# Kernel optimization log

Measured on AMD Instinct MI355X. Metric: run time of the kernel, lower is better.

Reference implementation:

```python
import jax, jax.numpy as jnp
import numpy as np

B, T, D, UNITS = 64, 1024, 512, 1024

def setup_inputs() -> dict:
    key = jax.random.key(0)
    ks = jax.random.split(key, 8)
    s = lambda fan_in: 1.0 / np.sqrt(fan_in)
    return {
        "features": jax.random.normal(ks[0], (B, T, D), dtype=jnp.float32),
        "hidden": jax.random.normal(ks[1], (B, D), dtype=jnp.float32),
        "W1_w": jax.random.normal(ks[2], (D, UNITS), dtype=jnp.float32) * s(D),
        "W1_b": jnp.zeros((UNITS,), dtype=jnp.float32),
        "W2_w": jax.random.normal(ks[3], (D, UNITS), dtype=jnp.float32) * s(D),
        "W2_b": jnp.zeros((UNITS,), dtype=jnp.float32),
        "V_w": jax.random.normal(ks[4], (UNITS, 1), dtype=jnp.float32) * s(UNITS),
        "V_b": jnp.zeros((1,), dtype=jnp.float32),
    }

def reference(features, hidden, W1_w, W1_b, W2_w, W2_b, V_w, V_b):
    # features: [B,T,D], hidden: [B,D]
    proj_f = jnp.einsum('btd,du->btu', features, W1_w) + W1_b          # [B,T,U]
    proj_h = (hidden @ W2_w + W2_b)[:, None, :]                        # [B,1,U]
    score = jnp.tanh(proj_f + proj_h)                                  # [B,T,U]
    logits = jnp.einsum('btu,uo->bto', score, V_w) + V_b               # [B,T,1]
    attention_weights = jax.nn.softmax(logits, axis=1)                 # [B,T,1]
    context_vector = jnp.sum(attention_weights * features, axis=1)     # [B,D]
    return context_vector, attention_weights
```

## Files before the change

### kernel.cpp

```cpp
#include <hip/hip_runtime.h>
#include <math.h>

#define B_ 64
#define T_ 1024
#define D_ 512
#define U_ 1024

typedef __bf16 bf16x8 __attribute__((ext_vector_type(8)));
typedef float f32x16 __attribute__((ext_vector_type(16)));
typedef unsigned int u32;

__device__ __forceinline__ float fast_tanh(float x) {
    float ax = fabsf(x);
    float e = __expf(2.0f * ax);
    float r = 1.0f - __fdividef(2.0f, e + 1.0f);
    return copysignf(r, x);
}

__device__ __forceinline__ u32 f2bf_pk(float lo, float hi) {
    u32 a = __float_as_uint(lo) + 0x8000u;
    u32 b = __float_as_uint(hi) + 0x8000u;
    return (a >> 16) | (b & 0xffff0000u);
}

__global__ __launch_bounds__(256) void prep_kernel(
    const float* __restrict__ W1, const float* __restrict__ hidden,
    const float* __restrict__ W2, const float* __restrict__ W2b,
    const float* __restrict__ W1b,
    unsigned short* __restrict__ W1F, float* __restrict__ ph,
    float* __restrict__ ctx0) {
    if (blockIdx.x < 256) {
        const int gid  = blockIdx.x * 256 + threadIdx.x;
        const int lane = gid & 63;
        const int frag = gid >> 6;
        const int ks = frag & 1;
        const int kt = (frag >> 1) & 15;
        const int ut = frag >> 5;
        const int u  = ut * 32 + (lane & 31);
        const int k0 = kt * 32 + ks * 16 + (lane >> 5) * 8;
        float f[8];
#pragma unroll
        for (int j = 0; j < 8; ++j) f[j] = W1[(size_t)(k0 + j) * U_ + u];
        uint4 w;
        w.x = f2bf_pk(f[0], f[1]);
        w.y = f2bf_pk(f[2], f[3]);
        w.z = f2bf_pk(f[4], f[5]);
        w.w = f2bf_pk(f[6], f[7]);
        *(uint4*)&W1F[(size_t)gid * 8] = w;
    } else {
        const int bx = blockIdx.x - 256;
        const int zi = bx * 256 + (int)threadIdx.x;
        if (zi < B_ * D_) ctx0[zi] = 0.f;
        const int u  = (bx & 3) * 256 + threadIdx.x;
        const int b  = bx >> 2;
        const float* h = hidden + b * D_;
        float acc = 0.f;
#pragma unroll 8
        for (int d = 0; d < D_; ++d) acc = fmaf(h[d], W2[(size_t)d * U_ + u], acc);
        ph[b * U_ + u] = acc + W2b[u] + W1b[u];
    }
}

__global__ __launch_bounds__(512, 4) void logits_mfma_kernel(
    const float* __restrict__ feat,
    const unsigned short* __restrict__ W1F,
    const float* __restrict__ ph,
    const float* __restrict__ Vw,
    float* __restrict__ lpart) {
    __shared__ __align__(16) char As[65536];

    const int tid  = threadIdx.x;
    const int tt   = blockIdx.x;
    const int b    = blockIdx.y;
    const int t0   = tt * 64;
    const int lane = tid & 63;
    const int widx = tid >> 6;
    const int l31 = lane & 31, g = lane >> 5;

    {
        const int r  = tid >> 3;
        const int s0 = tid & 7;
        const float* src = feat + ((size_t)(b * T_ + t0 + r)) * D_;
        const int xr = (r >> 2) & 3;
#pragma unroll
        for (int i = 0; i < 8; ++i) {
            const int s = s0 + 8 * i;
            const float4 v0 = *(const float4*)(src + s * 8);
            const float4 v1 = *(const float4*)(src + s * 8 + 4);
            uint4 w;
            w.x = f2bf_pk(v0.x, v0.y);
            w.y = f2bf_pk(v0.z, v0.w);
            w.z = f2bf_pk(v1.x, v1.y);
            w.w = f2bf_pk(v1.z, v1.w);
            const int panel = s >> 2, q = s & 3;
            *(uint4*)&As[panel * 4096 + r * 64 + (q ^ xr) * 16] = w;
        }
    }
    __syncthreads();

    const char* bb0 = (const char*)W1F + (size_t)(widx * 2) * 32768 + lane * 16;
    const char* bb1 = bb0 + (size_t)16 * 32768;

    f32x16 acc[2][2];
    bf16x8 b0[4], b1[4];

    auto loadB = [&](const char* bb, bf16x8* dst, int kt) {
#pragma unroll
        for (int nt = 0; nt < 2; ++nt)
#pragma unroll
            for (int ks = 0; ks < 2; ++ks)
                dst[nt * 2 + ks] =
                    *(const bf16x8*)(bb + nt * 32768 + (kt * 2 + ks) * 1024);
    };

    auto computeStep = [&](int kt, const bf16x8* bfr) {
        bf16x8 af[2][2];
#pragma unroll
        for (int ks = 0; ks < 2; ++ks)
#pragma unroll
            for (int mt = 0; mt < 2; ++mt) {
                const int rr = mt * 32 + l31;
                const int q  = (2 * ks + g) ^ ((rr >> 2) & 3);
                af[ks][mt] = *(const bf16x8*)&As[kt * 4096 + rr * 64 + q * 16];
            }
        __builtin_amdgcn_s_setprio(1);
#pragma unroll
        for (int ks = 0; ks < 2; ++ks)
#pragma unroll
            for (int mt = 0; mt < 2; ++mt)
#pragma unroll
                for (int nt = 0; nt < 2; ++nt)
                    acc[mt][nt] = __builtin_amdgcn_mfma_f32_32x32x16_bf16(
                        af[ks][mt], bfr[nt * 2 + ks], acc[mt][nt], 0, 0, 0);
        __builtin_amdgcn_s_setprio(0);
    };

    loadB(bb0, b0, 0);
#pragma unroll
    for (int uh = 0; uh < 2; ++uh) {
        const char* bb = uh ? bb1 : bb0;
#pragma unroll
        for (int mt = 0; mt < 2; ++mt)
#pragma unroll
            for (int nt = 0; nt < 2; ++nt) acc[mt][nt] = (f32x16)(0.f);

        for (int kt = 0; kt < 16; kt += 2) {
            loadB(bb, b1, kt + 1);
            computeStep(kt, b0);
            if (kt + 2 < 16) loadB(bb, b0, kt + 2);
            computeStep(kt + 1, b1);
        }
        if (uh == 0) loadB(bb1, b0, 0);

        float v[32];
#pragma unroll
        for (int i = 0; i < 32; ++i) v[i] = 0.f;

#pragma unroll
        for (int nt = 0; nt < 2; ++nt) {
            const int u = uh * 512 + widx * 64 + nt * 32 + l31;
            const float phv = ph[b * U_ + u];
            const float vw  = Vw[u];
#pragma unroll
            for (int mt = 0; mt < 2; ++mt)
#pragma unroll
                for (int r = 0; r < 16; ++r)
                    v[mt * 16 + r] =
                        fmaf(vw, fast_tanh(acc[mt][nt][r] + phv), v[mt * 16 + r]);
        }

#pragma unroll
        for (int s = 0; s < 5; ++s) {
            const int pb = 1 << s;
            const bool hi = (l31 & pb) != 0;
#pragma unroll
            for (int j = 0; j < (16 >> s); ++j) {
                const float a = v[2 * j];
                const float c = v[2 * j + 1];
                const float keep = hi ? c : a;
                const float send = hi ? a : c;
                v[j] = keep + __shfl_xor(send, pb);
            }
        }

        const int src = ((lane & 3) | (((lane >> 3) & 3) << 2) |
                         (((lane >> 5) & 1) << 4)) + 32 * ((lane >> 2) & 1);
        const float out = __shfl(v[0], src);
        lpart[((size_t)(uh * 8 + widx)) * (B_ * T_) + (size_t)b * T_ + t0 +
              lane] = out;
    }
}

__global__ __launch_bounds__(512) void ctx_kernel(
    const float* __restrict__ feat, const float* __restrict__ lpart,
    float* __restrict__ attn, float* __restrict__ ctx_out) {
    const int b   = blockIdx.y;
    const int seg = blockIdx.x;
    const int tid = threadIdx.x;
    __shared__ float wls[1024];
    __shared__ float redm[8];
    __shared__ float reds[8];

    float v[2];
    float mx = -3.4e38f;
#pragma unroll
    for (int j = 0; j < 2; ++j) {
        const int t = b * T_ + tid + 512 * j;
        float s0 = 0.f, s1 = 0.f;
#pragma unroll
        for (int sl = 0; sl < 8; ++sl) {
            s0 += lpart[(size_t)(2 * sl) * (B_ * T_) + t];
            s1 += lpart[(size_t)(2 * sl + 1) * (B_ * T_) + t];
        }
        v[j] = s0 + s1;
        mx = fmaxf(mx, v[j]);
    }
#pragma unroll
    for (int off = 32; off > 0; off >>= 1) mx = fmaxf(mx, __shfl_xor(mx, off));
    if ((tid & 63) == 0) redm[tid >> 6] = mx;
    __syncthreads();
    mx = fmaxf(fmaxf(fmaxf(redm[0], redm[1]), fmaxf(redm[2], redm[3])),
               fmaxf(fmaxf(redm[4], redm[5]), fmaxf(redm[6], redm[7])));
    float s = 0.f;
#pragma unroll
    for (int j = 0; j < 2; ++j) {
        v[j] = __expf(v[j] - mx);
        s += v[j];
    }
#pragma unroll
    for (int off = 32; off > 0; off >>= 1) s += __shfl_xor(s, off);
    if ((tid & 63) == 0) reds[tid >> 6] = s;
    __syncthreads();
    s = ((reds[0] + reds[1]) + (reds[2] + reds[3])) +
        ((reds[4] + reds[5]) + (reds[6] + reds[7]));
    const float inv = 1.0f / s;
    wls[tid]       = v[0] * inv;
    wls[tid + 512] = v[1] * inv;
    __syncthreads();

    if (tid < 128) attn[b * T_ + seg * 128 + tid] = wls[seg * 128 + tid];

    const int q  = tid >> 7;
    const int d4 = (tid & 127) * 4;
    const int t0 = seg * 128 + q * 32;
    const float* fb = feat + ((size_t)(b * T_ + t0)) * D_ + d4;
    const float* wb = &wls[t0];
    float4 acc = {0.f, 0.f, 0.f, 0.f};
#pragma unroll 4
    for (int t = 0; t < 32; ++t) {
        const float w  = wb[t];
        const float4 f = *(const float4*)&fb[(size_t)t * D_];
        acc.x = fmaf(w, f.x, acc.x);
        acc.y = fmaf(w, f.y, acc.y);
        acc.z = fmaf(w, f.z, acc.z);
        acc.w = fmaf(w, f.w, acc.w);
    }
    float* dst = ctx_out + b * D_ + d4;
    atomicAdd(dst + 0, acc.x);
    atomicAdd(dst + 1, acc.y);
    atomicAdd(dst + 2, acc.z);
    atomicAdd(dst + 3, acc.w);
}

extern "C" void kernel_launch(void* const* d_in, const int* in_sizes, int n_in,
                              void* d_out, int out_size, void* d_ws, size_t ws_size,
                              hipStream_t stream) {
    const float* feat   = (const float*)d_in[0];
    const float* hidden = (const float*)d_in[1];
    const float* W1w    = (const float*)d_in[2];
    const float* W1b    = (const float*)d_in[3];
    const float* W2w    = (const float*)d_in[4];
    const float* W2b    = (const float*)d_in[5];
    const float* Vw     = (const float*)d_in[6];

    float* out_ctx  = (float*)d_out;
    float* out_attn = out_ctx + B_ * D_;

    unsigned short* W1F = (unsigned short*)d_ws;
    float* ph     = (float*)(W1F + (size_t)U_ * D_);
    float* lpart  = ph + B_ * U_;

    prep_kernel<<<512, 256, 0, stream>>>(W1w, hidden, W2w, W2b, W1b, W1F, ph,
                                         out_ctx);
    logits_mfma_kernel<<<dim3(16, B_), 512, 0, stream>>>(feat, W1F, ph, Vw,
                                                         lpart);
    ctx_kernel<<<dim3(8, B_), 512, 0, stream>>>(feat, lpart, out_attn, out_ctx);
}
```

Measured before the change: 344.2 us.

## Split logits kernel across unit halves and pre-reduce context partials in LDS

```diff
diff --git a/kernel.cpp b/kernel.cpp
--- a/kernel.cpp
+++ b/kernel.cpp
@@ -70,7 +70,9 @@
     __shared__ __align__(16) char As[65536];
 
     const int tid  = threadIdx.x;
-    const int tt   = blockIdx.x;
+    const int gx   = blockIdx.x;
+    const int uh   = gx & 1;
+    const int tt   = gx >> 1;
     const int b    = blockIdx.y;
     const int t0   = tt * 64;
     const int lane = tid & 63;
@@ -98,19 +100,19 @@
     }
     __syncthreads();
 
-    const char* bb0 = (const char*)W1F + (size_t)(widx * 2) * 32768 + lane * 16;
-    const char* bb1 = bb0 + (size_t)16 * 32768;
+    const char* bfbase = (const char*)W1F +
+                         (size_t)((uh * 16 + widx * 2)) * 32768 + lane * 16;
 
     f32x16 acc[2][2];
     bf16x8 b0[4], b1[4];
 
-    auto loadB = [&](const char* bb, bf16x8* dst, int kt) {
+    auto loadB = [&](bf16x8* dst, int kt) {
 #pragma unroll
         for (int nt = 0; nt < 2; ++nt)
 #pragma unroll
             for (int ks = 0; ks < 2; ++ks)
                 dst[nt * 2 + ks] =
-                    *(const bf16x8*)(bb + nt * 32768 + (kt * 2 + ks) * 1024);
+                    *(const bf16x8*)(bfbase + nt * 32768 + (kt * 2 + ks) * 1024);
     };
 
     auto computeStep = [&](int kt, const bf16x8* bfr) {
@@ -135,60 +137,55 @@
         __builtin_amdgcn_s_setprio(0);
     };
 
-    loadB(bb0, b0, 0);
-#pragma unroll
-    for (int uh = 0; uh < 2; ++uh) {
-        const char* bb = uh ? bb1 : bb0;
+#pragma unroll
+    for (int mt = 0; mt < 2; ++mt)
+#pragma unroll
+        for (int nt = 0; nt < 2; ++nt) acc[mt][nt] = (f32x16)(0.f);
+
+    loadB(b0, 0);
+    for (int kt = 0; kt < 16; kt += 2) {
+        loadB(b1, kt + 1);
+        computeStep(kt, b0);
+        if (kt + 2 < 16) loadB(b0, kt + 2);
+        computeStep(kt + 1, b1);
+    }
+
+    float v[32];
+#pragma unroll
+    for (int i = 0; i < 32; ++i) v[i] = 0.f;
+
+#pragma unroll
+    for (int nt = 0; nt < 2; ++nt) {
+        const int u = uh * 512 + widx * 64 + nt * 32 + l31;
+        const float phv = ph[b * U_ + u];
+        const float vw  = Vw[u];
 #pragma unroll
         for (int mt = 0; mt < 2; ++mt)
 #pragma unroll
-            for (int nt = 0; nt < 2; ++nt) acc[mt][nt] = (f32x16)(0.f);
-
-        for (int kt = 0; kt < 16; kt += 2) {
-            loadB(bb, b1, kt + 1);
-            computeStep(kt, b0);
-            if (kt + 2 < 16) loadB(bb, b0, kt + 2);
-            computeStep(kt + 1, b1);
+            for (int r = 0; r < 16; ++r)
+                v[mt * 16 + r] =
+                    fmaf(vw, fast_tanh(acc[mt][nt][r] + phv), v[mt * 16 + r]);
+    }
+
+#pragma unroll
+    for (int s = 0; s < 5; ++s) {
+        const int pb = 1 << s;
+        const bool hi = (l31 & pb) != 0;
+#pragma unroll
+        for (int j = 0; j < (16 >> s); ++j) {
+            const float a = v[2 * j];
+            const float c = v[2 * j + 1];
+            const float keep = hi ? c : a;
+            const float send = hi ? a : c;
+            v[j] = keep + __shfl_xor(send, pb);
         }
-        if (uh == 0) loadB(bb1, b0, 0);
-
-        float v[32];
-#pragma unroll
-        for (int i = 0; i < 32; ++i) v[i] = 0.f;
-
-#pragma unroll
-        for (int nt = 0; nt < 2; ++nt) {
-            const int u = uh * 512 + widx * 64 + nt * 32 + l31;
-            const float phv = ph[b * U_ + u];
-            const float vw  = Vw[u];
-#pragma unroll
-            for (int mt = 0; mt < 2; ++mt)
-#pragma unroll
-                for (int r = 0; r < 16; ++r)
-                    v[mt * 16 + r] =
-                        fmaf(vw, fast_tanh(acc[mt][nt][r] + phv), v[mt * 16 + r]);
-        }
-
-#pragma unroll
-        for (int s = 0; s < 5; ++s) {
-            const int pb = 1 << s;
-            const bool hi = (l31 & pb) != 0;
-#pragma unroll
-            for (int j = 0; j < (16 >> s); ++j) {
-                const float a = v[2 * j];
-                const float c = v[2 * j + 1];
-                const float keep = hi ? c : a;
-                const float send = hi ? a : c;
-                v[j] = keep + __shfl_xor(send, pb);
-            }
-        }
-
-        const int src = ((lane & 3) | (((lane >> 3) & 3) << 2) |
-                         (((lane >> 5) & 1) << 4)) + 32 * ((lane >> 2) & 1);
-        const float out = __shfl(v[0], src);
-        lpart[((size_t)(uh * 8 + widx)) * (B_ * T_) + (size_t)b * T_ + t0 +
-              lane] = out;
-    }
+    }
+
+    const int src = ((lane & 3) | (((lane >> 3) & 3) << 2) |
+                     (((lane >> 5) & 1) << 4)) + 32 * ((lane >> 2) & 1);
+    const float out = __shfl(v[0], src);
+    lpart[((size_t)(uh * 8 + widx)) * (B_ * T_) + (size_t)b * T_ + t0 + lane] =
+        out;
 }
 
 __global__ __launch_bounds__(512) void ctx_kernel(
@@ -200,6 +197,7 @@
     __shared__ float wls[1024];
     __shared__ float redm[8];
     __shared__ float reds[8];
+    __shared__ __align__(16) float4 cp[512];
 
     float v[2];
     float mx = -3.4e38f;
@@ -255,11 +253,19 @@
         acc.z = fmaf(w, f.z, acc.z);
         acc.w = fmaf(w, f.w, acc.w);
     }
-    float* dst = ctx_out + b * D_ + d4;
-    atomicAdd(dst + 0, acc.x);
-    atomicAdd(dst + 1, acc.y);
-    atomicAdd(dst + 2, acc.z);
-    atomicAdd(dst + 3, acc.w);
+    cp[tid] = acc;
+    __syncthreads();
+    if (tid < 128) {
+        const float4 a0 = cp[tid];
+        const float4 a1 = cp[tid + 128];
+        const float4 a2 = cp[tid + 256];
+        const float4 a3 = cp[tid + 384];
+        float* dst = ctx_out + b * D_ + tid * 4;
+        atomicAdd(dst + 0, (a0.x + a1.x) + (a2.x + a3.x));
+        atomicAdd(dst + 1, (a0.y + a1.y) + (a2.y + a3.y));
+        atomicAdd(dst + 2, (a0.z + a1.z) + (a2.z + a3.z));
+        atomicAdd(dst + 3, (a0.w + a1.w) + (a2.w + a3.w));
+    }
 }
 
 extern "C" void kernel_launch(void* const* d_in, const int* in_sizes, int n_in,
@@ -282,7 +288,7 @@
 
     prep_kernel<<<512, 256, 0, stream>>>(W1w, hidden, W2w, W2b, W1b, W1F, ph,
                                          out_ctx);
-    logits_mfma_kernel<<<dim3(16, B_), 512, 0, stream>>>(feat, W1F, ph, Vw,
+    logits_mfma_kernel<<<dim3(32, B_), 512, 0, stream>>>(feat, W1F, ph, Vw,
                                                          lpart);
     ctx_kernel<<<dim3(8, B_), 512, 0, stream>>>(feat, lpart, out_attn, out_ctx);
 }
```

Result: faster. 326.2 us (-5.2%).
